# Kernel optimization log

Measured on AMD Instinct MI355X. Metric: run time of the kernel, lower is better.

## Reference

```python
import jax, jax.numpy as jnp
import numpy as np

EPS = 1e-5
NEG_SLOPE = 0.1


def _gcn_layer(x, row, col, W, b):
    # GCNConv, improved=True (self-loop weight 2.0), symmetric normalization.
    N = x.shape[0]
    xw = x @ W                                   # [N, H]
    ew = jnp.ones(row.shape[0], dtype=x.dtype)   # edge_weight=None -> ones
    deg = jax.ops.segment_sum(ew, col, num_segments=N) + 2.0  # +2 from improved self loop
    dinv = jax.lax.rsqrt(deg)                    # deg >= 2, always finite
    norm = dinv[row] * dinv[col]                 # [E]
    agg = jax.ops.segment_sum(norm[:, None] * xw[row], col, num_segments=N)
    agg = agg + (2.0 * dinv * dinv)[:, None] * xw  # self-loop contribution
    return agg + b


def _batchnorm(x, w, b):
    # training-mode BN over node dim (biased variance), eps=1e-5
    mu = jnp.mean(x, axis=0)
    var = jnp.mean((x - mu) ** 2, axis=0)
    return (x - mu) * jax.lax.rsqrt(var + EPS) * w + b


def setup_inputs() -> dict:
    key = jax.random.key(0)
    ks = jax.random.split(key, 10)
    N, E, F, H, OUT, G = 100000, 800000, 128, 128, 128, 2048
    x = jax.random.normal(ks[0], (N, F), dtype=jnp.float32)
    edge_index = jax.random.randint(ks[1], (2, E), 0, N, dtype=jnp.int64)
    batch = jnp.sort(jax.random.randint(ks[2], (N,), 0, G, dtype=jnp.int64))
    s1 = 1.0 / np.sqrt(F)
    s2 = 1.0 / np.sqrt(H)
    return {
        "x": x,
        "edge_index": edge_index,
        "batch": batch,
        "W1": jax.random.uniform(ks[3], (F, H), jnp.float32, -s1, s1),
        "b1": jnp.zeros((H,), jnp.float32),
        "bn1_w": jnp.ones((H,), jnp.float32),
        "bn1_b": jnp.zeros((H,), jnp.float32),
        "W2": jax.random.uniform(ks[4], (H, H), jnp.float32, -s2, s2),
        "b2": jnp.zeros((H,), jnp.float32),
        "bn2_w": jnp.ones((H,), jnp.float32),
        "bn2_b": jnp.zeros((H,), jnp.float32),
        "Wf": jax.random.uniform(ks[5], (H, OUT), jnp.float32, -s2, s2),
        "bf": jax.random.uniform(ks[6], (OUT,), jnp.float32, -s2, s2),
        "num_graphs": G,
    }


def reference(x, edge_index, batch, W1, b1, bn1_w, bn1_b, W2, b2, bn2_w, bn2_b, Wf, bf, num_graphs):
    row, col = edge_index[0], edge_index[1]
    h = _gcn_layer(x, row, col, W1, b1)
    h = jax.nn.leaky_relu(_batchnorm(h, bn1_w, bn1_b), NEG_SLOPE)
    # dropout omitted (deterministic reference / eval mode)
    h = _gcn_layer(h, row, col, W2, b2)
    h = jax.nn.leaky_relu(_batchnorm(h, bn2_w, bn2_b), NEG_SLOPE)
    pooled = jax.ops.segment_max(h, batch, num_segments=num_graphs)  # [G, H]
    pooled = jnp.where(jnp.isneginf(pooled), 0.0, pooled)            # empty graphs -> 0
    return pooled @ Wf + bf
```

## Files before the change

### kernel.cpp

```cpp
#include <hip/hip_runtime.h>
#include <hip/hip_bf16.h>

#define EPSV 1e-5f
#define SLOPE 0.1f

typedef __attribute__((ext_vector_type(8))) unsigned short ushort8v;
typedef __attribute__((ext_vector_type(8))) short bf16x8;
typedef __attribute__((ext_vector_type(4))) float f32x4;

static __device__ inline unsigned short f2bf(float f) {
    __hip_bfloat16 b = __float2bfloat16(f);
    return *reinterpret_cast<unsigned short*>(&b);
}
static __device__ inline float bf2f(unsigned short u) {
    return __uint_as_float(((unsigned)u) << 16);
}

__global__ __launch_bounds__(256) void k_count(const int* __restrict__ col,
                                               unsigned* __restrict__ cnt, int E) {
    int e = blockIdx.x * 256 + threadIdx.x;
    if (e < E) atomicAdd(&cnt[col[e]], 1u);
}

__global__ __launch_bounds__(256) void k_chunk_sum(const unsigned* __restrict__ cnt, int N,
                                                   unsigned* __restrict__ bsum,
                                                   float* __restrict__ dinv) {
    __shared__ unsigned ls[256];
    int base = blockIdx.x * 1024;
    unsigned s = 0;
    for (int i = threadIdx.x; i < 1024; i += 256) {
        int idx = base + i;
        if (idx < N) {
            unsigned c = cnt[idx];
            s += c;
            dinv[idx] = rsqrtf((float)c + 2.0f);
        }
    }
    ls[threadIdx.x] = s;
    __syncthreads();
    for (int st = 128; st > 0; st >>= 1) {
        if (threadIdx.x < st) ls[threadIdx.x] += ls[threadIdx.x + st];
        __syncthreads();
    }
    if (threadIdx.x == 0) bsum[blockIdx.x] = ls[0];
}

__global__ __launch_bounds__(128) void k_scan_bsum(unsigned* __restrict__ bsum, int nb) {
    const int t = threadIdx.x;
    unsigned v = (t < nb) ? bsum[t] : 0u;
    unsigned s = v;
    for (int d = 1; d < 64; d <<= 1) {
        unsigned y = __shfl_up(s, d, 64);
        if ((t & 63) >= d) s += y;
    }
    __shared__ unsigned wtot;
    if (t == 63) wtot = s;
    __syncthreads();
    unsigned base = (t >= 64) ? wtot : 0u;
    if (t < nb) bsum[t] = base + s - v;
}

__global__ __launch_bounds__(256) void k_scan_chunks(const unsigned* __restrict__ cnt, int N,
                                                     const unsigned* __restrict__ bsum,
                                                     int* __restrict__ off,
                                                     int* __restrict__ cursor, int E) {
    __shared__ unsigned ls[256];
    int base = blockIdx.x * 1024;
    unsigned v[4];
    unsigned s = 0;
#pragma unroll
    for (int j = 0; j < 4; j++) {
        int idx = base + threadIdx.x * 4 + j;
        v[j] = (idx < N) ? cnt[idx] : 0u;
        s += v[j];
    }
    ls[threadIdx.x] = s;
    __syncthreads();
    if (threadIdx.x == 0) {
        unsigned acc = bsum[blockIdx.x];
        for (int i = 0; i < 256; i++) { unsigned t = ls[i]; ls[i] = acc; acc += t; }
    }
    __syncthreads();
    unsigned acc = ls[threadIdx.x];
#pragma unroll
    for (int j = 0; j < 4; j++) {
        int idx = base + threadIdx.x * 4 + j;
        if (idx < N) { off[idx] = (int)acc; cursor[idx] = (int)acc; }
        acc += v[j];
    }
    if (base + threadIdx.x * 4 <= N - 1 && N - 1 < base + threadIdx.x * 4 + 4) off[N] = E;
}

__global__ __launch_bounds__(256) void k_place(const int* __restrict__ row,
                                               const int* __restrict__ col,
                                               const float* __restrict__ dinv,
                                               int* __restrict__ cursor,
                                               int2* __restrict__ spack, int E) {
    int e = blockIdx.x * 256 + threadIdx.x;
    if (e >= E) return;
    int r = row[e], c = col[e];
    int pos = atomicAdd(&cursor[c], 1);
    spack[pos] = make_int2(r, __float_as_int(dinv[r] * dinv[c]));
}

__global__ __launch_bounds__(256) void k_prepw(const float* __restrict__ W1,
                                               const float* __restrict__ W2,
                                               const float* __restrict__ Wf,
                                               unsigned short* __restrict__ wT) {
    int m = blockIdx.x >> 4;
    int idx = (blockIdx.x & 15) * 256 + threadIdx.x;
    const float* W = (m == 0) ? W1 : (m == 1) ? W2 : Wf;
    unsigned short* T = wT + (size_t)m * 16384;
    int k = idx >> 5, n4 = (idx & 31) * 4;
    float4 v = *(const float4*)(W + (size_t)k * 128 + n4);
    T[(size_t)(n4 + 0) * 128 + k] = f2bf(v.x);
    T[(size_t)(n4 + 1) * 128 + k] = f2bf(v.y);
    T[(size_t)(n4 + 2) * 128 + k] = f2bf(v.z);
    T[(size_t)(n4 + 3) * 128 + k] = f2bf(v.w);
}

template <int MODE>
__global__ __launch_bounds__(256) void k_gemm_m(const void* __restrict__ Xv,
                                                const unsigned short* __restrict__ wT,
                                                const float* __restrict__ sums, float invN,
                                                const float* __restrict__ bnw,
                                                const float* __restrict__ bnb,
                                                const float* __restrict__ bias,
                                                void* __restrict__ Yv, int N) {
    __shared__ unsigned short xs[64][136];
    __shared__ float sc[128], sb[128];
    const int tid = threadIdx.x;
    if (MODE == 1) {
        if (tid < 128) {
            float mu = sums[tid] * invN;
            float var = sums[128 + tid] * invN - mu * mu;
            float s = rsqrtf(var + EPSV) * bnw[tid];
            sc[tid] = s;
            sb[tid] = bnb[tid] - mu * s;
        }
        __syncthreads();
    }
    const int base = blockIdx.x * 64;
    if (MODE == 1) {
        const unsigned short* Xh = (const unsigned short*)Xv;
        for (int i = tid; i < 1024; i += 256) {
            int r = i >> 4, c8 = (i & 15) * 8;
            int row = base + r; if (row >= N) row = N - 1;
            ushort8v v = *(const ushort8v*)(Xh + (size_t)row * 128 + c8);
            ushort8v o;
#pragma unroll
            for (int j = 0; j < 8; j++) {
                float f = fmaf(bf2f(v[j]), sc[c8 + j], sb[c8 + j]);
                f = f > 0.f ? f : SLOPE * f;
                o[j] = f2bf(f);
            }
            *(ushort8v*)(&xs[r][c8]) = o;
        }
    } else {
        const float* X = (const float*)Xv;
        for (int i = tid; i < 2048; i += 256) {
            int r = i >> 5, c4 = i & 31;
            int row = base + r; if (row >= N) row = N - 1;
            float4 v = ((const float4*)(X + (size_t)row * 128))[c4];
            ushort4 o;
            o.x = f2bf(v.x); o.y = f2bf(v.y); o.z = f2bf(v.z); o.w = f2bf(v.w);
            *(ushort4*)(&xs[r][c4 * 4]) = o;
        }
    }
    __syncthreads();

    const int lane = tid & 63;
    const int m0 = (tid >> 6) * 16;
    const int mr = lane & 15;
    const int kg = lane >> 4;
    f32x4 acc[8];
#pragma unroll
    for (int nf = 0; nf < 8; nf++) acc[nf] = (f32x4){0.f, 0.f, 0.f, 0.f};

#pragma unroll
    for (int kt = 0; kt < 4; kt++) {
        bf16x8 a = *(const bf16x8*)(&xs[m0 + mr][kt * 32 + kg * 8]);
#pragma unroll
        for (int nf = 0; nf < 8; nf++) {
            bf16x8 b = *(const bf16x8*)(wT + (size_t)(nf * 16 + mr) * 128 + kt * 32 + kg * 8);
            acc[nf] = __builtin_amdgcn_mfma_f32_16x16x32_bf16(a, b, acc[nf], 0, 0, 0);
        }
    }

    if (MODE == 2) {
#pragma unroll
        for (int nf = 0; nf < 8; nf++) {
#pragma unroll
            for (int r = 0; r < 4; r++) {
                int row = base + m0 + kg * 4 + r;
                if (row < N) {
                    int coln = nf * 16 + mr;
                    ((float*)Yv)[(size_t)row * 128 + coln] = acc[nf][r] + bias[coln];
                }
            }
        }
    } else {
        __syncthreads();
#pragma unroll
        for (int nf = 0; nf < 8; nf++) {
#pragma unroll
            for (int r = 0; r < 4; r++) {
                xs[m0 + kg * 4 + r][nf * 16 + mr] = f2bf(acc[nf][r]);
            }
        }
        __syncthreads();
        unsigned short* Yh = (unsigned short*)Yv;
        for (int i = tid; i < 1024; i += 256) {
            int r = i >> 4, c8 = (i & 15) * 8;
            int row = base + r;
            if (row < N)
                *(ushort8v*)(Yh + (size_t)row * 128 + c8) = *(const ushort8v*)(&xs[r][c8]);
        }
    }
}

__global__ __launch_bounds__(256) void k_agg5(const unsigned short* __restrict__ xwh,
                                              const int* __restrict__ off,
                                              const int2* __restrict__ spack,
                                              const float* __restrict__ dinv,
                                              const float* __restrict__ bias,
                                              unsigned short* __restrict__ h,
                                              float* __restrict__ sums, int N) {
    __shared__ float ls1[128], ls2[128];
    const int tid = threadIdx.x;
    if (tid < 128) { ls1[tid] = 0.f; ls2[tid] = 0.f; }
    __syncthreads();

    const int q = tid & 15;
    const int grp = (blockIdx.x * 256 + tid) >> 4;
    const int nGrp = gridDim.x * 16;

    float bj[8];
#pragma unroll
    for (int j = 0; j < 8; j++) bj[j] = bias[q * 8 + j];
    float st1[8] = {0, 0, 0, 0, 0, 0, 0, 0};
    float st2[8] = {0, 0, 0, 0, 0, 0, 0, 0};

    for (int n = grp; n < N; n += nGrp) {
        const int s = off[n], e = off[n + 1];
        float a[8] = {0, 0, 0, 0, 0, 0, 0, 0};
        int i = s;
        for (; i + 8 <= e; i += 8) {
            int2 p0 = spack[i + 0], p1 = spack[i + 1], p2 = spack[i + 2], p3 = spack[i + 3];
            int2 p4 = spack[i + 4], p5 = spack[i + 5], p6 = spack[i + 6], p7 = spack[i + 7];
            ushort8v v0 = *(const ushort8v*)(xwh + (size_t)p0.x * 128 + q * 8);
            ushort8v v1 = *(const ushort8v*)(xwh + (size_t)p1.x * 128 + q * 8);
            ushort8v v2 = *(const ushort8v*)(xwh + (size_t)p2.x * 128 + q * 8);
            ushort8v v3 = *(const ushort8v*)(xwh + (size_t)p3.x * 128 + q * 8);
            ushort8v v4 = *(const ushort8v*)(xwh + (size_t)p4.x * 128 + q * 8);
            ushort8v v5 = *(const ushort8v*)(xwh + (size_t)p5.x * 128 + q * 8);
            ushort8v v6 = *(const ushort8v*)(xwh + (size_t)p6.x * 128 + q * 8);
            ushort8v v7 = *(const ushort8v*)(xwh + (size_t)p7.x * 128 + q * 8);
            float n0 = __int_as_float(p0.y), n1 = __int_as_float(p1.y);
            float n2 = __int_as_float(p2.y), n3 = __int_as_float(p3.y);
            float n4 = __int_as_float(p4.y), n5 = __int_as_float(p5.y);
            float n6 = __int_as_float(p6.y), n7 = __int_as_float(p7.y);
#pragma unroll
            for (int j = 0; j < 8; j++) {
                float t = fmaf(n0, bf2f(v0[j]), fmaf(n1, bf2f(v1[j]),
                          fmaf(n2, bf2f(v2[j]), n3 * bf2f(v3[j]))));
                float u = fmaf(n4, bf2f(v4[j]), fmaf(n5, bf2f(v5[j]),
                          fmaf(n6, bf2f(v6[j]), n7 * bf2f(v7[j]))));
                a[j] += t + u;
            }
        }
        for (; i + 4 <= e; i += 4) {
            int2 p0 = spack[i + 0], p1 = spack[i + 1], p2 = spack[i + 2], p3 = spack[i + 3];
            ushort8v v0 = *(const ushort8v*)(xwh + (size_t)p0.x * 128 + q * 8);
            ushort8v v1 = *(const ushort8v*)(xwh + (size_t)p1.x * 128 + q * 8);
            ushort8v v2 = *(const ushort8v*)(xwh + (size_t)p2.x * 128 + q * 8);
            ushort8v v3 = *(const ushort8v*)(xwh + (size_t)p3.x * 128 + q * 8);
            float n0 = __int_as_float(p0.y), n1 = __int_as_float(p1.y);
            float n2 = __int_as_float(p2.y), n3 = __int_as_float(p3.y);
#pragma unroll
            for (int j = 0; j < 8; j++) {
                a[j] += fmaf(n0, bf2f(v0[j]), fmaf(n1, bf2f(v1[j]),
                        fmaf(n2, bf2f(v2[j]), n3 * bf2f(v3[j]))));
            }
        }
        for (; i < e; ++i) {
            int2 p = spack[i];
            ushort8v v = *(const ushort8v*)(xwh + (size_t)p.x * 128 + q * 8);
            float nm = __int_as_float(p.y);
#pragma unroll
            for (int j = 0; j < 8; j++) a[j] = fmaf(nm, bf2f(v[j]), a[j]);
        }
        float dc = dinv[n];
        float sl = 2.f * dc * dc;
        ushort8v xv = *(const ushort8v*)(xwh + (size_t)n * 128 + q * 8);
        ushort8v ov;
#pragma unroll
        for (int j = 0; j < 8; j++) {
            float o = fmaf(sl, bf2f(xv[j]), a[j]) + bj[j];
            st1[j] += o;
            st2[j] += o * o;
            ov[j] = f2bf(o);
        }
        *(ushort8v*)(h + (size_t)n * 128 + q * 8) = ov;
    }
#pragma unroll
    for (int j = 0; j < 8; j++) {
        atomicAdd(&ls1[q * 8 + j], st1[j]);
        atomicAdd(&ls2[q * 8 + j], st2[j]);
    }
    __syncthreads();
    if (tid < 128) {
        atomicAdd(&sums[tid], ls1[tid]);
        atomicAdd(&sums[128 + tid], ls2[tid]);
    }
}

__global__ __launch_bounds__(256) void k_pool_init(unsigned* __restrict__ p, int total) {
    int i = blockIdx.x * 256 + threadIdx.x;
    if (i < total) p[i] = 0x007FFFFFu;
}

__device__ inline unsigned enc_f(float x) {
    unsigned u = __float_as_uint(x);
    return (u & 0x80000000u) ? ~u : (u | 0x80000000u);
}

__global__ __launch_bounds__(256) void k_pool2(const unsigned short* __restrict__ h,
                                               const int* __restrict__ batch,
                                               const float* __restrict__ sums, float invN,
                                               const float* __restrict__ bnw,
                                               const float* __restrict__ bnb,
                                               unsigned* __restrict__ pooled, int N) {
    const int f = threadIdx.x & 127;
    const int half = threadIdx.x >> 7;
    float mu = sums[f] * invN;
    float var = sums[128 + f] * invN - mu * mu;
    float scale = rsqrtf(var + EPSV) * bnw[f];
    float bias = bnb[f] - mu * scale;
    const int base = blockIdx.x * 128;
    const int end = min(base + 128, N);
    float m = -__builtin_inff();
    int g = -1;
    for (int n = base + half; n < end; n += 2) {
        int bg = batch[n];
        if (bg != g) {
            if (g >= 0) atomicMax(&pooled[(size_t)g * 128 + f], enc_f(m));
            g = bg;
            m = -__builtin_inff();
        }
        float v = fmaf(bf2f(h[(size_t)n * 128 + f]), scale, bias);
        v = v > 0.f ? v : SLOPE * v;
        m = fmaxf(m, v);
    }
    if (g >= 0) atomicMax(&pooled[(size_t)g * 128 + f], enc_f(m));
}

__global__ __launch_bounds__(256) void k_decode(unsigned* __restrict__ p, int total) {
    int i = blockIdx.x * 256 + threadIdx.x;
    if (i >= total) return;
    unsigned u = p[i];
    float v;
    if (u == 0x007FFFFFu) v = 0.f;
    else if (u & 0x80000000u) v = __uint_as_float(u & 0x7FFFFFFFu);
    else v = __uint_as_float(~u);
    p[i] = __float_as_uint(v);
}

extern "C" void kernel_launch(void* const* d_in, const int* in_sizes, int n_in,
                              void* d_out, int out_size, void* d_ws, size_t ws_size,
                              hipStream_t stream) {
    const float* x     = (const float*)d_in[0];
    const int*   ei    = (const int*)d_in[1];
    const int*   batch = (const int*)d_in[2];
    const float* W1    = (const float*)d_in[3];
    const float* b1    = (const float*)d_in[4];
    const float* bn1w  = (const float*)d_in[5];
    const float* bn1b  = (const float*)d_in[6];
    const float* W2    = (const float*)d_in[7];
    const float* b2    = (const float*)d_in[8];
    const float* bn2w  = (const float*)d_in[9];
    const float* bn2b  = (const float*)d_in[10];
    const float* Wf    = (const float*)d_in[11];
    const float* bf    = (const float*)d_in[12];

    const int N = in_sizes[0] / 128;
    const int E = in_sizes[1] / 2;
    const int G = out_size / 128;
    const int* rowp = ei;
    const int* colp = ei + E;
    float* out = (float*)d_out;
    const float invN = 1.0f / N;

    char* w = (char*)d_ws;
    unsigned short* bufAh = (unsigned short*)w; w += (size_t)N * 128 * 2;
    unsigned short* bufBh = (unsigned short*)w; w += (size_t)N * 128 * 2;
    float*    dinv   = (float*)w;    w += (size_t)N * 4;
    unsigned* cnt    = (unsigned*)w; w += (size_t)N * 4;
    int*      cursor = (int*)w;      w += (size_t)N * 4;
    int*      off    = (int*)w;      w += (size_t)(N + 4) * 4;
    unsigned* bsum   = (unsigned*)w; w += 1024 * 4;
    int2*     spack  = (int2*)w;     w += (size_t)E * 8;
    float*    sums   = (float*)w;    w += 512 * 4;
    unsigned* pooled = (unsigned*)w; w += (size_t)G * 128 * 4;
    unsigned short* wT = (unsigned short*)w; w += 3 * 16384 * 2;

    float* sums1 = sums;
    float* sums2 = sums + 256;
    const int nb = (N + 1023) / 1024;

    hipMemsetAsync(cnt, 0, (size_t)N * 4, stream);
    hipMemsetAsync(sums, 0, 512 * 4, stream);
    k_prepw<<<48, 256, 0, stream>>>(W1, W2, Wf, wT);
    k_count<<<(E + 255) / 256, 256, 0, stream>>>(colp, cnt, E);
    k_chunk_sum<<<nb, 256, 0, stream>>>(cnt, N, bsum, dinv);
    k_scan_bsum<<<1, 128, 0, stream>>>(bsum, nb);
    k_scan_chunks<<<nb, 256, 0, stream>>>(cnt, N, bsum, off, cursor, E);
    k_place<<<(E + 255) / 256, 256, 0, stream>>>(rowp, colp, dinv, cursor, spack, E);

    const int aggBlocks = 2048;
    const int gemmGrid = (N + 63) / 64;

    k_gemm_m<0><<<gemmGrid, 256, 0, stream>>>(x, wT, nullptr, 0.f, nullptr, nullptr,
                                              nullptr, bufAh, N);
    k_agg5<<<aggBlocks, 256, 0, stream>>>(bufAh, off, spack, dinv, b1, bufBh, sums1, N);

    k_gemm_m<1><<<gemmGrid, 256, 0, stream>>>(bufBh, wT + 16384, sums1, invN, bn1w, bn1b,
                                              nullptr, bufAh, N);
    k_agg5<<<aggBlocks, 256, 0, stream>>>(bufAh, off, spack, dinv, b2, bufBh, sums2, N);

    k_pool_init<<<(G * 128 + 255) / 256, 256, 0, stream>>>(pooled, G * 128);
    k_pool2<<<(N + 127) / 128, 256, 0, stream>>>(bufBh, batch, sums2, invN, bn2w, bn2b,
                                                 pooled, N);
    k_decode<<<(G * 128 + 255) / 256, 256, 0, stream>>>(pooled, G * 128);

    k_gemm_m<2><<<(G + 63) / 64, 256, 0, stream>>>((const float*)pooled, wT + 32768,
                                                   nullptr, 0.f, nullptr, nullptr, bf,
                                                   out, G);
}
```

Before: 441.1 us.

## Fuse pooling, decode and final linear into one per-graph tail kernel; nontemporal gathers

Replaces the pool init, atomic-max pooling, decode and MFMA final GEMM with a single kernel. Each wavefront owns one graph, binary-searches the sorted batch array for its node range, and computes the BN+leaky-relu max directly. It then applies the Wf linear layer with shuffles in fp32, which removes three launches and the atomics. Separately, the aggregation gathers switch to nontemporal loads, which risks losing L2 reuse of the gathered xw rows. The fused tail also runs one wave per graph serially over nodes, which may cost parallelism.

Measured after the change: 452.2 us. 1.03x slower.

```diff
diff --git a/kernel.cpp b/kernel.cpp
--- a/kernel.cpp
+++ b/kernel.cpp
@@ -7,6 +7,7 @@
 typedef __attribute__((ext_vector_type(8))) unsigned short ushort8v;
 typedef __attribute__((ext_vector_type(8))) short bf16x8;
 typedef __attribute__((ext_vector_type(4))) float f32x4;
+typedef __attribute__((ext_vector_type(4))) unsigned int uint4v;
 
 static __device__ inline unsigned short f2bf(float f) {
     __hip_bfloat16 b = __float2bfloat16(f);
@@ -14,6 +15,10 @@
 }
 static __device__ inline float bf2f(unsigned short u) {
     return __uint_as_float(((unsigned)u) << 16);
+}
+static __device__ inline ushort8v ntload8(const unsigned short* p) {
+    uint4v t = __builtin_nontemporal_load((const uint4v*)p);
+    return *reinterpret_cast<ushort8v*>(&t);
 }
 
 __global__ __launch_bounds__(256) void k_count(const int* __restrict__ col,
@@ -105,11 +110,10 @@
 
 __global__ __launch_bounds__(256) void k_prepw(const float* __restrict__ W1,
                                                const float* __restrict__ W2,
-                                               const float* __restrict__ Wf,
                                                unsigned short* __restrict__ wT) {
     int m = blockIdx.x >> 4;
     int idx = (blockIdx.x & 15) * 256 + threadIdx.x;
-    const float* W = (m == 0) ? W1 : (m == 1) ? W2 : Wf;
+    const float* W = (m == 0) ? W1 : W2;
     unsigned short* T = wT + (size_t)m * 16384;
     int k = idx >> 5, n4 = (idx & 31) * 4;
     float4 v = *(const float4*)(W + (size_t)k * 128 + n4);
@@ -125,7 +129,6 @@
                                                 const float* __restrict__ sums, float invN,
                                                 const float* __restrict__ bnw,
                                                 const float* __restrict__ bnb,
-                                                const float* __restrict__ bias,
                                                 void* __restrict__ Yv, int N) {
     __shared__ unsigned short xs[64][136];
     __shared__ float sc[128], sb[128];
@@ -187,35 +190,21 @@
         }
     }
 
-    if (MODE == 2) {
-#pragma unroll
-        for (int nf = 0; nf < 8; nf++) {
-#pragma unroll
-            for (int r = 0; r < 4; r++) {
-                int row = base + m0 + kg * 4 + r;
-                if (row < N) {
-                    int coln = nf * 16 + mr;
-                    ((float*)Yv)[(size_t)row * 128 + coln] = acc[nf][r] + bias[coln];
-                }
-            }
-        }
-    } else {
-        __syncthreads();
-#pragma unroll
-        for (int nf = 0; nf < 8; nf++) {
-#pragma unroll
-            for (int r = 0; r < 4; r++) {
-                xs[m0 + kg * 4 + r][nf * 16 + mr] = f2bf(acc[nf][r]);
-            }
-        }
-        __syncthreads();
-        unsigned short* Yh = (unsigned short*)Yv;
-        for (int i = tid; i < 1024; i += 256) {
-            int r = i >> 4, c8 = (i & 15) * 8;
-            int row = base + r;
-            if (row < N)
-                *(ushort8v*)(Yh + (size_t)row * 128 + c8) = *(const ushort8v*)(&xs[r][c8]);
-        }
+    __syncthreads();
+#pragma unroll
+    for (int nf = 0; nf < 8; nf++) {
+#pragma unroll
+        for (int r = 0; r < 4; r++) {
+            xs[m0 + kg * 4 + r][nf * 16 + mr] = f2bf(acc[nf][r]);
+        }
+    }
+    __syncthreads();
+    unsigned short* Yh = (unsigned short*)Yv;
+    for (int i = tid; i < 1024; i += 256) {
+        int r = i >> 4, c8 = (i & 15) * 8;
+        int row = base + r;
+        if (row < N)
+            *(ushort8v*)(Yh + (size_t)row * 128 + c8) = *(const ushort8v*)(&xs[r][c8]);
     }
 }
 
@@ -248,14 +237,14 @@
         for (; i + 8 <= e; i += 8) {
             int2 p0 = spack[i + 0], p1 = spack[i + 1], p2 = spack[i + 2], p3 = spack[i + 3];
             int2 p4 = spack[i + 4], p5 = spack[i + 5], p6 = spack[i + 6], p7 = spack[i + 7];
-            ushort8v v0 = *(const ushort8v*)(xwh + (size_t)p0.x * 128 + q * 8);
-            ushort8v v1 = *(const ushort8v*)(xwh + (size_t)p1.x * 128 + q * 8);
-            ushort8v v2 = *(const ushort8v*)(xwh + (size_t)p2.x * 128 + q * 8);
-            ushort8v v3 = *(const ushort8v*)(xwh + (size_t)p3.x * 128 + q * 8);
-            ushort8v v4 = *(const ushort8v*)(xwh + (size_t)p4.x * 128 + q * 8);
-            ushort8v v5 = *(const ushort8v*)(xwh + (size_t)p5.x * 128 + q * 8);
-            ushort8v v6 = *(const ushort8v*)(xwh + (size_t)p6.x * 128 + q * 8);
-            ushort8v v7 = *(const ushort8v*)(xwh + (size_t)p7.x * 128 + q * 8);
+            ushort8v v0 = ntload8(xwh + (size_t)p0.x * 128 + q * 8);
+            ushort8v v1 = ntload8(xwh + (size_t)p1.x * 128 + q * 8);
+            ushort8v v2 = ntload8(xwh + (size_t)p2.x * 128 + q * 8);
+            ushort8v v3 = ntload8(xwh + (size_t)p3.x * 128 + q * 8);
+            ushort8v v4 = ntload8(xwh + (size_t)p4.x * 128 + q * 8);
+            ushort8v v5 = ntload8(xwh + (size_t)p5.x * 128 + q * 8);
+            ushort8v v6 = ntload8(xwh + (size_t)p6.x * 128 + q * 8);
+            ushort8v v7 = ntload8(xwh + (size_t)p7.x * 128 + q * 8);
             float n0 = __int_as_float(p0.y), n1 = __int_as_float(p1.y);
             float n2 = __int_as_float(p2.y), n3 = __int_as_float(p3.y);
             float n4 = __int_as_float(p4.y), n5 = __int_as_float(p5.y);
@@ -271,10 +260,10 @@
         }
         for (; i + 4 <= e; i += 4) {
             int2 p0 = spack[i + 0], p1 = spack[i + 1], p2 = spack[i + 2], p3 = spack[i + 3];
-            ushort8v v0 = *(const ushort8v*)(xwh + (size_t)p0.x * 128 + q * 8);
-            ushort8v v1 = *(const ushort8v*)(xwh + (size_t)p1.x * 128 + q * 8);
-            ushort8v v2 = *(const ushort8v*)(xwh + (size_t)p2.x * 128 + q * 8);
-            ushort8v v3 = *(const ushort8v*)(xwh + (size_t)p3.x * 128 + q * 8);
+            ushort8v v0 = ntload8(xwh + (size_t)p0.x * 128 + q * 8);
+            ushort8v v1 = ntload8(xwh + (size_t)p1.x * 128 + q * 8);
+            ushort8v v2 = ntload8(xwh + (size_t)p2.x * 128 + q * 8);
+            ushort8v v3 = ntload8(xwh + (size_t)p3.x * 128 + q * 8);
             float n0 = __int_as_float(p0.y), n1 = __int_as_float(p1.y);
             float n2 = __int_as_float(p2.y), n3 = __int_as_float(p3.y);
 #pragma unroll
@@ -285,7 +274,7 @@
         }
         for (; i < e; ++i) {
             int2 p = spack[i];
-            ushort8v v = *(const ushort8v*)(xwh + (size_t)p.x * 128 + q * 8);
+            ushort8v v = ntload8(xwh + (size_t)p.x * 128 + q * 8);
             float nm = __int_as_float(p.y);
 #pragma unroll
             for (int j = 0; j < 8; j++) a[j] = fmaf(nm, bf2f(v[j]), a[j]);
@@ -315,55 +304,55 @@
     }
 }
 
-__global__ __launch_bounds__(256) void k_pool_init(unsigned* __restrict__ p, int total) {
-    int i = blockIdx.x * 256 + threadIdx.x;
-    if (i < total) p[i] = 0x007FFFFFu;
-}
-
-__device__ inline unsigned enc_f(float x) {
-    unsigned u = __float_as_uint(x);
-    return (u & 0x80000000u) ? ~u : (u | 0x80000000u);
-}
-
-__global__ __launch_bounds__(256) void k_pool2(const unsigned short* __restrict__ h,
-                                               const int* __restrict__ batch,
-                                               const float* __restrict__ sums, float invN,
-                                               const float* __restrict__ bnw,
-                                               const float* __restrict__ bnb,
-                                               unsigned* __restrict__ pooled, int N) {
-    const int f = threadIdx.x & 127;
-    const int half = threadIdx.x >> 7;
-    float mu = sums[f] * invN;
-    float var = sums[128 + f] * invN - mu * mu;
-    float scale = rsqrtf(var + EPSV) * bnw[f];
-    float bias = bnb[f] - mu * scale;
-    const int base = blockIdx.x * 128;
-    const int end = min(base + 128, N);
-    float m = -__builtin_inff();
-    int g = -1;
-    for (int n = base + half; n < end; n += 2) {
-        int bg = batch[n];
-        if (bg != g) {
-            if (g >= 0) atomicMax(&pooled[(size_t)g * 128 + f], enc_f(m));
-            g = bg;
-            m = -__builtin_inff();
-        }
-        float v = fmaf(bf2f(h[(size_t)n * 128 + f]), scale, bias);
-        v = v > 0.f ? v : SLOPE * v;
-        m = fmaxf(m, v);
-    }
-    if (g >= 0) atomicMax(&pooled[(size_t)g * 128 + f], enc_f(m));
-}
-
-__global__ __launch_bounds__(256) void k_decode(unsigned* __restrict__ p, int total) {
-    int i = blockIdx.x * 256 + threadIdx.x;
-    if (i >= total) return;
-    unsigned u = p[i];
-    float v;
-    if (u == 0x007FFFFFu) v = 0.f;
-    else if (u & 0x80000000u) v = __uint_as_float(u & 0x7FFFFFFFu);
-    else v = __uint_as_float(~u);
-    p[i] = __float_as_uint(v);
+__global__ __launch_bounds__(256) void k_tail(const unsigned short* __restrict__ h,
+                                              const int* __restrict__ batch,
+                                              const float* __restrict__ sums, float invN,
+                                              const float* __restrict__ bnw,
+                                              const float* __restrict__ bnb,
+                                              const float* __restrict__ Wf,
+                                              const float* __restrict__ bf,
+                                              float* __restrict__ out, int N, int G) {
+    const int lane = threadIdx.x & 63;
+    const int g = blockIdx.x * 4 + (threadIdx.x >> 6);
+    if (g >= G) return;
+    const int f0 = lane, f1 = lane + 64;
+    float mu0 = sums[f0] * invN;
+    float var0 = sums[128 + f0] * invN - mu0 * mu0;
+    float sc0 = rsqrtf(var0 + EPSV) * bnw[f0];
+    float sb0 = bnb[f0] - mu0 * sc0;
+    float mu1 = sums[f1] * invN;
+    float var1 = sums[128 + f1] * invN - mu1 * mu1;
+    float sc1 = rsqrtf(var1 + EPSV) * bnw[f1];
+    float sb1 = bnb[f1] - mu1 * sc1;
+
+    int lo, hi;
+    { int a = 0, b = N; while (a < b) { int m = (a + b) >> 1; if (batch[m] < g) a = m + 1; else b = m; } lo = a; }
+    { int a = lo, b = N; while (a < b) { int m = (a + b) >> 1; if (batch[m] < g + 1) a = m + 1; else b = m; } hi = a; }
+
+    float m0 = -__builtin_inff(), m1 = -__builtin_inff();
+    for (int n = lo; n < hi; n++) {
+        float v0 = fmaf(bf2f(h[(size_t)n * 128 + f0]), sc0, sb0);
+        float v1 = fmaf(bf2f(h[(size_t)n * 128 + f1]), sc1, sb1);
+        v0 = v0 > 0.f ? v0 : SLOPE * v0;
+        v1 = v1 > 0.f ? v1 : SLOPE * v1;
+        m0 = fmaxf(m0, v0);
+        m1 = fmaxf(m1, v1);
+    }
+    if (lo >= hi) { m0 = 0.f; m1 = 0.f; }
+
+    float o0 = bf[f0], o1 = bf[f1];
+    for (int k = 0; k < 64; k++) {
+        float vk = __shfl(m0, k, 64);
+        o0 = fmaf(vk, Wf[(size_t)k * 128 + f0], o0);
+        o1 = fmaf(vk, Wf[(size_t)k * 128 + f1], o1);
+    }
+    for (int k = 0; k < 64; k++) {
+        float vk = __shfl(m1, k, 64);
+        o0 = fmaf(vk, Wf[(size_t)(k + 64) * 128 + f0], o0);
+        o1 = fmaf(vk, Wf[(size_t)(k + 64) * 128 + f1], o1);
+    }
+    out[(size_t)g * 128 + f0] = o0;
+    out[(size_t)g * 128 + f1] = o1;
 }
 
 extern "C" void kernel_launch(void* const* d_in, const int* in_sizes, int n_in,
@@ -401,8 +390,7 @@
     unsigned* bsum   = (unsigned*)w; w += 1024 * 4;
     int2*     spack  = (int2*)w;     w += (size_t)E * 8;
     float*    sums   = (float*)w;    w += 512 * 4;
-    unsigned* pooled = (unsigned*)w; w += (size_t)G * 128 * 4;
-    unsigned short* wT = (unsigned short*)w; w += 3 * 16384 * 2;
+    unsigned short* wT = (unsigned short*)w; w += 2 * 16384 * 2;
 
     float* sums1 = sums;
     float* sums2 = sums + 256;
@@ -410,7 +398,7 @@
 
     hipMemsetAsync(cnt, 0, (size_t)N * 4, stream);
     hipMemsetAsync(sums, 0, 512 * 4, stream);
-    k_prepw<<<48, 256, 0, stream>>>(W1, W2, Wf, wT);
+    k_prepw<<<32, 256, 0, stream>>>(W1, W2, wT);
     k_count<<<(E + 255) / 256, 256, 0, stream>>>(colp, cnt, E);
     k_chunk_sum<<<nb, 256, 0, stream>>>(cnt, N, bsum, dinv);
     k_scan_bsum<<<1, 128, 0, stream>>>(bsum, nb);
@@ -421,19 +409,13 @@
     const int gemmGrid = (N + 63) / 64;
 
     k_gemm_m<0><<<gemmGrid, 256, 0, stream>>>(x, wT, nullptr, 0.f, nullptr, nullptr,
-                                              nullptr, bufAh, N);
+                                              bufAh, N);
     k_agg5<<<aggBlocks, 256, 0, stream>>>(bufAh, off, spack, dinv, b1, bufBh, sums1, N);
 
     k_gemm_m<1><<<gemmGrid, 256, 0, stream>>>(bufBh, wT + 16384, sums1, invN, bn1w, bn1b,
-                                              nullptr, bufAh, N);
+                                              bufAh, N);
     k_agg5<<<aggBlocks, 256, 0, stream>>>(bufAh, off, spack, dinv, b2, bufBh, sums2, N);
 
-    k_pool_init<<<(G * 128 + 255) / 256, 256, 0, stream>>>(pooled, G * 128);
-    k_pool2<<<(N + 127) / 128, 256, 0, stream>>>(bufBh, batch, sums2, invN, bn2w, bn2b,
-                                                 pooled, N);
-    k_decode<<<(G * 128 + 255) / 256, 256, 0, stream>>>(pooled, G * 128);
-
-    k_gemm_m<2><<<(G + 63) / 64, 256, 0, stream>>>((const float*)pooled, wT + 32768,
-                                                   nullptr, 0.f, nullptr, nullptr, bf,
-                                                   out, G);
-}
+    k_tail<<<(G + 3) / 4, 256, 0, stream>>>(bufBh, batch, sums2, invN, bn2w, bn2b,
+                                            Wf, bf, out, N, G);
+}
```
